# Optimization experiments

Hardware: AMD Instinct MI355X
Metric: run time of the kernel (lower is better)

The kernel has to match this reference:

```python
import math
import jax, jax.numpy as jnp
import numpy as np

EMBED_DIM = 1024
NUM_HEADS = 16
HEAD_DIM = EMBED_DIM // NUM_HEADS  # 64


def setup_inputs() -> dict:
    key = jax.random.key(0)
    kx, kq, ko = jax.random.split(key, 3)
    B, S, D = 4, 1024, EMBED_DIM
    x = jax.random.normal(kx, (B, S, D), dtype=jnp.float32)
    # xavier_uniform for Dense kernels, zeros for biases
    def xavier(k, shape):
        fan_in, fan_out = shape[0], shape[1]
        limit = math.sqrt(6.0 / (fan_in + fan_out))
        return jax.random.uniform(k, shape, jnp.float32, -limit, limit)
    W_qkv = xavier(kq, (D, 3 * D))
    b_qkv = jnp.zeros((3 * D,), jnp.float32)
    W_o = xavier(ko, (D, D))
    b_o = jnp.zeros((D,), jnp.float32)
    return {"x": x, "W_qkv": W_qkv, "b_qkv": b_qkv, "W_o": W_o, "b_o": b_o}


def reference(x, W_qkv, b_qkv, W_o, b_o):
    B, S, D = x.shape
    H, hd = NUM_HEADS, HEAD_DIM
    qkv = x @ W_qkv + b_qkv                         # [B,S,3D]
    qkv = qkv.reshape(B, S, H, 3 * hd).transpose(0, 2, 1, 3)  # [B,H,S,3hd]
    q, k, v = jnp.split(qkv, 3, axis=-1)            # each [B,H,S,hd]
    attn_logits = jnp.einsum('bhqd,bhkd->bhqk', q, k) / math.sqrt(hd)
    attention = jax.nn.softmax(attn_logits, axis=-1)  # [B,H,S,S]
    values = jnp.einsum('bhqk,bhkd->bhqd', attention, v)
    values = values.transpose(0, 2, 1, 3).reshape(B, S, D)
    o = values @ W_o + b_o
    return (o, attention)
```

## Files before the change

kernel.cpp:

```cpp
#include <hip/hip_runtime.h>

#define B_   4
#define S_   1024
#define D_   1024
#define H_   16
#define HD_  64

typedef __bf16 bf16_t;
typedef __attribute__((ext_vector_type(8))) __bf16 bf16x8;
typedef __attribute__((ext_vector_type(4))) float f32x4;

#define MFMA16(a, b, c) __builtin_amdgcn_mfma_f32_16x16x32_bf16((a), (b), (c), 0, 0, 0)

__device__ inline unsigned short f2bf(float f) {
    unsigned int u = __builtin_bit_cast(unsigned int, f);
    u += 0x7FFFu + ((u >> 16) & 1u);
    return (unsigned short)(u >> 16);
}

__device__ inline bf16x8 ld_frag(const unsigned short* p) {
    uint4 u = *(const uint4*)p;
    return __builtin_bit_cast(bf16x8, u);
}

__global__ __launch_bounds__(256) void convert_f32_bf16(
    const float* __restrict__ in, unsigned short* __restrict__ out)
{
    const size_t idx = (size_t)blockIdx.x * 256 + threadIdx.x;
    float4 v = *(const float4*)(in + idx * 4);
    unsigned short* o = out + idx * 4;
    ushort4 r;
    r.x = f2bf(v.x); r.y = f2bf(v.y); r.z = f2bf(v.z); r.w = f2bf(v.w);
    *(ushort4*)o = r;
}

__global__ __launch_bounds__(256) void transpose_f32_bf16(
    const float* __restrict__ in, unsigned short* __restrict__ out,
    int K, int N)
{
    __shared__ float T[64][65];
    const int tid = threadIdx.x;
    const int k0 = blockIdx.y * 64, n0 = blockIdx.x * 64;
#pragma unroll
    for (int i = 0; i < 4; ++i) {
        int c = tid + i * 256;
        int row = c >> 4, col = (c & 15) << 2;
        float4 v = *(const float4*)(in + (size_t)(k0 + row) * N + n0 + col);
        T[row][col + 0] = v.x; T[row][col + 1] = v.y;
        T[row][col + 2] = v.z; T[row][col + 3] = v.w;
    }
    __syncthreads();
#pragma unroll
    for (int i = 0; i < 4; ++i) {
        int c = tid + i * 256;
        int nr = c >> 4, kc = (c & 15) << 2;
        ushort4 r;
        r.x = f2bf(T[kc + 0][nr]); r.y = f2bf(T[kc + 1][nr]);
        r.z = f2bf(T[kc + 2][nr]); r.w = f2bf(T[kc + 3][nr]);
        *(ushort4*)(out + (size_t)(n0 + nr) * K + k0 + kc) = r;
    }
}

template<int MODE>
__global__ __launch_bounds__(256) void gemm_bf16(
    const unsigned short* __restrict__ A,
    const unsigned short* __restrict__ Bt,
    const float* __restrict__ bias,
    unsigned short* __restrict__ qk,
    unsigned short* __restrict__ vt,
    float* __restrict__ out,
    int K, int N)
{
    __shared__ unsigned short Alds[128][72];
    __shared__ unsigned short Blds[128][72];
    const int tid  = threadIdx.x;
    const int l    = tid & 63, w = tid >> 6;
    const int wm   = w >> 1, wn = w & 1;
    const int quad = l >> 4, n16 = l & 15;
    const int bm = blockIdx.y * 128, bn = blockIdx.x * 128;

    const f32x4 zero4 = {0.f, 0.f, 0.f, 0.f};
    f32x4 acc[4][4];
#pragma unroll
    for (int i = 0; i < 4; ++i)
#pragma unroll
        for (int j = 0; j < 4; ++j) acc[i][j] = zero4;

    for (int k0 = 0; k0 < K; k0 += 64) {
#pragma unroll
        for (int i = 0; i < 4; ++i) {
            int c = tid + i * 256;
            int row = c >> 3, off = (c & 7) << 3;
            *(uint4*)&Alds[row][off] = *(const uint4*)(A + (size_t)(bm + row) * K + k0 + off);
            *(uint4*)&Blds[row][off] = *(const uint4*)(Bt + (size_t)(bn + row) * K + k0 + off);
        }
        __syncthreads();
#pragma unroll
        for (int kk = 0; kk < 2; ++kk) {
            const int kc = kk * 32 + quad * 8;
            bf16x8 af[4], bfv[4];
#pragma unroll
            for (int i = 0; i < 4; ++i) af[i]  = ld_frag(&Alds[wm * 64 + i * 16 + n16][kc]);
#pragma unroll
            for (int j = 0; j < 4; ++j) bfv[j] = ld_frag(&Blds[wn * 64 + j * 16 + n16][kc]);
#pragma unroll
            for (int i = 0; i < 4; ++i)
#pragma unroll
                for (int j = 0; j < 4; ++j)
                    acc[i][j] = MFMA16(af[i], bfv[j], acc[i][j]);
        }
        __syncthreads();
    }

#pragma unroll
    for (int j = 0; j < 4; ++j) {
        const int col0 = bn + wn * 64 + j * 16;
        const int col  = col0 + n16;
        const float bv = bias ? bias[col] : 0.f;
        if (MODE == 0) {
            const int head = col0 / 192;
            const int rem  = col0 % 192;
            if (rem < 128) {
#pragma unroll
                for (int i = 0; i < 4; ++i)
#pragma unroll
                    for (int r = 0; r < 4; ++r) {
                        int row = bm + wm * 64 + i * 16 + quad * 4 + r;
                        qk[(size_t)row * 2048 + head * 128 + rem + n16] =
                            f2bf(acc[i][j][r] + bv);
                    }
            } else {
                const int dim = rem - 128 + n16;
#pragma unroll
                for (int i = 0; i < 4; ++i)
#pragma unroll
                    for (int r = 0; r < 4; ++r) {
                        int row = bm + wm * 64 + i * 16 + quad * 4 + r;
                        vt[(size_t)(((row >> 10) << 4) + head) * 65536 +
                           (size_t)dim * 1024 + (row & 1023)] =
                            f2bf(acc[i][j][r] + bv);
                    }
            }
        } else {
#pragma unroll
            for (int i = 0; i < 4; ++i)
#pragma unroll
                for (int r = 0; r < 4; ++r) {
                    int row = bm + wm * 64 + i * 16 + quad * 4 + r;
                    out[(size_t)row * N + col] = acc[i][j][r] + bv;
                }
        }
    }
}

__global__ __launch_bounds__(256) void attn_fused(
    const unsigned short* __restrict__ qk,
    const unsigned short* __restrict__ vt,
    float* __restrict__ attn,
    unsigned short* __restrict__ values)
{
    __shared__ unsigned short Klds[64][72];
    __shared__ unsigned short Vlds[64][72];
    __shared__ unsigned short Plds[16][1032];
    __shared__ float redbuf[2][4][16];

    const int qb = blockIdx.x, bh = blockIdx.y;
    const int b = bh >> 4, h = bh & 15;
    const int tid = threadIdx.x, l = tid & 63, w = tid >> 6;
    const int quad = l >> 4, n16 = l & 15;

    bf16x8 qf[2];
    {
        const unsigned short* qbase =
            qk + (size_t)(b * 1024 + qb * 16 + n16) * 2048 + h * 128 + quad * 8;
        qf[0] = ld_frag(qbase);
        qf[1] = ld_frag(qbase + 32);
    }

    const f32x4 zero4 = {0.f, 0.f, 0.f, 0.f};
    f32x4 c[16];
#pragma unroll
    for (int s = 0; s < 16; ++s) c[s] = zero4;

    const unsigned short* kbase = qk + (size_t)(b * 1024) * 2048 + h * 128 + 64;
    for (int s = 0; s < 16; ++s) {
#pragma unroll
        for (int i = 0; i < 2; ++i) {
            int cc = tid + i * 256;
            int key = cc >> 3, off = (cc & 7) << 3;
            *(uint4*)&Klds[key][off] =
                *(const uint4*)(kbase + (size_t)(s * 64 + key) * 2048 + off);
        }
        __syncthreads();
        const int krow = w * 16 + n16;
        bf16x8 k0f = ld_frag(&Klds[krow][quad * 8]);
        bf16x8 k1f = ld_frag(&Klds[krow][32 + quad * 8]);
        c[s] = MFMA16(qf[0], k0f, c[s]);
        c[s] = MFMA16(qf[1], k1f, c[s]);
        __syncthreads();
    }

    float mx[4] = {-1e30f, -1e30f, -1e30f, -1e30f};
#pragma unroll
    for (int s = 0; s < 16; ++s)
#pragma unroll
        for (int r = 0; r < 4; ++r) {
            c[s][r] *= 0.125f;
            mx[r] = fmaxf(mx[r], c[s][r]);
        }
#pragma unroll
    for (int off = 1; off <= 8; off <<= 1)
#pragma unroll
        for (int r = 0; r < 4; ++r)
            mx[r] = fmaxf(mx[r], __shfl_xor(mx[r], off, 64));
    if (n16 == 0)
#pragma unroll
        for (int r = 0; r < 4; ++r) redbuf[0][w][quad * 4 + r] = mx[r];
    __syncthreads();
#pragma unroll
    for (int r = 0; r < 4; ++r) {
        const int row = quad * 4 + r;
        float m = redbuf[0][0][row];
        m = fmaxf(m, redbuf[0][1][row]);
        m = fmaxf(m, redbuf[0][2][row]);
        m = fmaxf(m, redbuf[0][3][row]);
        mx[r] = m;
    }

    float sm[4] = {0.f, 0.f, 0.f, 0.f};
#pragma unroll
    for (int s = 0; s < 16; ++s)
#pragma unroll
        for (int r = 0; r < 4; ++r) {
            float e = __expf(c[s][r] - mx[r]);
            c[s][r] = e;
            sm[r] += e;
        }
#pragma unroll
    for (int off = 1; off <= 8; off <<= 1)
#pragma unroll
        for (int r = 0; r < 4; ++r)
            sm[r] += __shfl_xor(sm[r], off, 64);
    if (n16 == 0)
#pragma unroll
        for (int r = 0; r < 4; ++r) redbuf[1][w][quad * 4 + r] = sm[r];
    __syncthreads();
    float inv[4];
#pragma unroll
    for (int r = 0; r < 4; ++r) {
        const int row = quad * 4 + r;
        inv[r] = 1.f / (redbuf[1][0][row] + redbuf[1][1][row] +
                        redbuf[1][2][row] + redbuf[1][3][row]);
    }

    float* abase = attn + ((size_t)bh * 1024 + qb * 16) * 1024;
#pragma unroll
    for (int s = 0; s < 16; ++s)
#pragma unroll
        for (int r = 0; r < 4; ++r) {
            const float a = c[s][r] * inv[r];
            const int row = quad * 4 + r;
            const int key = s * 64 + w * 16 + n16;
            abase[(size_t)row * 1024 + key] = a;
            Plds[row][key] = f2bf(a);
        }

    f32x4 o = zero4;
    const unsigned short* vbase = vt + (size_t)bh * 65536;
    for (int s = 0; s < 16; ++s) {
#pragma unroll
        for (int i = 0; i < 2; ++i) {
            int cc = tid + i * 256;
            int dim = cc >> 3, off = (cc & 7) << 3;
            *(uint4*)&Vlds[dim][off] =
                *(const uint4*)(vbase + (size_t)dim * 1024 + s * 64 + off);
        }
        __syncthreads();
#pragma unroll
        for (int kk = 0; kk < 2; ++kk) {
            bf16x8 pf = ld_frag(&Plds[n16][s * 64 + kk * 32 + quad * 8]);
            bf16x8 vf = ld_frag(&Vlds[w * 16 + n16][kk * 32 + quad * 8]);
            o = MFMA16(pf, vf, o);
        }
        __syncthreads();
    }

#pragma unroll
    for (int r = 0; r < 4; ++r) {
        const int row = quad * 4 + r;
        values[(size_t)(b * 1024 + qb * 16 + row) * 1024 + h * 64 + w * 16 + n16] =
            f2bf(o[r]);
    }
}

extern "C" void kernel_launch(void* const* d_in, const int* in_sizes, int n_in,
                              void* d_out, int out_size, void* d_ws, size_t ws_size,
                              hipStream_t stream)
{
    const float* x     = (const float*)d_in[0];
    const float* W_qkv = (const float*)d_in[1];
    const float* b_qkv = (const float*)d_in[2];
    const float* W_o   = (const float*)d_in[3];
    const float* b_o   = (const float*)d_in[4];

    float* o_out    = (float*)d_out;
    float* attn_out = o_out + (size_t)B_ * S_ * D_;

    const size_t M1 = 1ull << 20;
    unsigned short* ws      = (unsigned short*)d_ws;
    unsigned short* x_bf    = ws;
    unsigned short* wqkvt   = ws + 4 * M1;
    unsigned short* wot     = ws + 7 * M1;
    unsigned short* qkbuf   = ws + 8 * M1;
    unsigned short* vtbuf   = ws + 16 * M1;
    unsigned short* valbuf  = ws + 20 * M1;

    convert_f32_bf16<<<4096, 256, 0, stream>>>(x, x_bf);
    transpose_f32_bf16<<<dim3(3072 / 64, 1024 / 64), 256, 0, stream>>>(W_qkv, wqkvt, 1024, 3072);
    transpose_f32_bf16<<<dim3(1024 / 64, 1024 / 64), 256, 0, stream>>>(W_o, wot, 1024, 1024);

    gemm_bf16<0><<<dim3(3072 / 128, 4096 / 128), 256, 0, stream>>>(
        x_bf, wqkvt, b_qkv, qkbuf, vtbuf, nullptr, 1024, 3072);

    attn_fused<<<dim3(S_ / 16, B_ * H_), 256, 0, stream>>>(
        qkbuf, vtbuf, attn_out, valbuf);

    gemm_bf16<1><<<dim3(1024 / 128, 4096 / 128), 256, 0, stream>>>(
        valbuf, wot, b_o, nullptr, nullptr, o_out, 1024, 1024);
}
```

Measured before the change: 477.4 us.

## Use direct global-to-LDS loads in GEMM, double-buffer K/V, split V transpose

The GEMM tile loads now use global_load_lds to write global memory straight into LDS, which removes the register staging and drops the padded LDS rows. The QKV GEMM writes V in its natural layout, and a separate small kernel transposes it into the V^T layout, replacing the scattered strided stores in the GEMM epilogue. The attention kernel double-buffers its K and V tiles so that loading the next tile overlaps compute on the current one, with one barrier per iteration instead of two. The risks are LDS bank conflicts from the unpadded GEMM tiles, an extra kernel launch with its own memory pass for V, and valbuf being reused as scratch for V before the attention kernel overwrites it.

```diff
diff --git a/kernel.cpp b/kernel.cpp
--- a/kernel.cpp
+++ b/kernel.cpp
@@ -21,6 +21,13 @@
 __device__ inline bf16x8 ld_frag(const unsigned short* p) {
     uint4 u = *(const uint4*)p;
     return __builtin_bit_cast(bf16x8, u);
+}
+
+__device__ inline void gload_lds16(const unsigned short* g, unsigned short* l) {
+    __builtin_amdgcn_global_load_lds(
+        (const __attribute__((address_space(1))) void*)g,
+        (__attribute__((address_space(3))) void*)l,
+        16, 0, 0);
 }
 
 __global__ __launch_bounds__(256) void convert_f32_bf16(
@@ -61,24 +68,53 @@
     }
 }
 
+__global__ __launch_bounds__(256) void transpose_v_bf16(
+    const unsigned short* __restrict__ v,
+    unsigned short* __restrict__ vt)
+{
+    __shared__ unsigned short T[64][65];
+    const int tid = threadIdx.x;
+    const int kt = blockIdx.x, bh = blockIdx.y;
+    const int b = bh >> 4, h = bh & 15;
+#pragma unroll
+    for (int i = 0; i < 2; ++i) {
+        const int c = tid + i * 256;
+        const int key = c >> 3, off = (c & 7) << 3;
+        uint4 u = *(const uint4*)(v + (size_t)(b * 1024 + kt * 64 + key) * 1024 + h * 64 + off);
+        union { uint4 u4; unsigned short us[8]; } uu; uu.u4 = u;
+#pragma unroll
+        for (int t = 0; t < 8; ++t) T[key][off + t] = uu.us[t];
+    }
+    __syncthreads();
+#pragma unroll
+    for (int i = 0; i < 16; ++i) {
+        const int c = tid + i * 256;
+        const int dim = c >> 6, key = c & 63;
+        vt[((size_t)bh * 64 + dim) * 1024 + kt * 64 + key] = T[key][dim];
+    }
+}
+
 template<int MODE>
 __global__ __launch_bounds__(256) void gemm_bf16(
     const unsigned short* __restrict__ A,
     const unsigned short* __restrict__ Bt,
     const float* __restrict__ bias,
     unsigned short* __restrict__ qk,
-    unsigned short* __restrict__ vt,
+    unsigned short* __restrict__ vnat,
     float* __restrict__ out,
     int K, int N)
 {
-    __shared__ unsigned short Alds[128][72];
-    __shared__ unsigned short Blds[128][72];
+    __shared__ unsigned short Alds[128][64];
+    __shared__ unsigned short Blds[128][64];
     const int tid  = threadIdx.x;
     const int l    = tid & 63, w = tid >> 6;
     const int wm   = w >> 1, wn = w & 1;
     const int quad = l >> 4, n16 = l & 15;
     const int bm = blockIdx.y * 128, bn = blockIdx.x * 128;
 
+    const int lrow = l >> 3;
+    const int lcol = (l & 7) << 3;
+
     const f32x4 zero4 = {0.f, 0.f, 0.f, 0.f};
     f32x4 acc[4][4];
 #pragma unroll
@@ -89,10 +125,10 @@
     for (int k0 = 0; k0 < K; k0 += 64) {
 #pragma unroll
         for (int i = 0; i < 4; ++i) {
-            int c = tid + i * 256;
-            int row = c >> 3, off = (c & 7) << 3;
-            *(uint4*)&Alds[row][off] = *(const uint4*)(A + (size_t)(bm + row) * K + k0 + off);
-            *(uint4*)&Blds[row][off] = *(const uint4*)(Bt + (size_t)(bn + row) * K + k0 + off);
+            const int c8  = (w * 4 + i) * 8;
+            const int row = c8 + lrow;
+            gload_lds16(A  + (size_t)(bm + row) * K + k0 + lcol, &Alds[c8][0]);
+            gload_lds16(Bt + (size_t)(bn + row) * K + k0 + lcol, &Blds[c8][0]);
         }
         __syncthreads();
 #pragma unroll
@@ -130,15 +166,13 @@
                             f2bf(acc[i][j][r] + bv);
                     }
             } else {
-                const int dim = rem - 128 + n16;
+                const int dcol = head * 64 + (rem - 128) + n16;
 #pragma unroll
                 for (int i = 0; i < 4; ++i)
 #pragma unroll
                     for (int r = 0; r < 4; ++r) {
                         int row = bm + wm * 64 + i * 16 + quad * 4 + r;
-                        vt[(size_t)(((row >> 10) << 4) + head) * 65536 +
-                           (size_t)dim * 1024 + (row & 1023)] =
-                            f2bf(acc[i][j][r] + bv);
+                        vnat[(size_t)row * 1024 + dcol] = f2bf(acc[i][j][r] + bv);
                     }
             }
         } else {
@@ -159,8 +193,7 @@
     float* __restrict__ attn,
     unsigned short* __restrict__ values)
 {
-    __shared__ unsigned short Klds[64][72];
-    __shared__ unsigned short Vlds[64][72];
+    __shared__ unsigned short KV[2][64][72];
     __shared__ unsigned short Plds[16][1032];
     __shared__ float redbuf[2][4][16];
 
@@ -168,6 +201,9 @@
     const int b = bh >> 4, h = bh & 15;
     const int tid = threadIdx.x, l = tid & 63, w = tid >> 6;
     const int quad = l >> 4, n16 = l & 15;
+
+    const int skey = tid >> 3;
+    const int soff = (tid & 7) << 3;
 
     bf16x8 qf[2];
     {
@@ -183,18 +219,23 @@
     for (int s = 0; s < 16; ++s) c[s] = zero4;
 
     const unsigned short* kbase = qk + (size_t)(b * 1024) * 2048 + h * 128 + 64;
+#pragma unroll
+    for (int i = 0; i < 2; ++i)
+        *(uint4*)&KV[0][skey + i * 32][soff] =
+            *(const uint4*)(kbase + (size_t)(skey + i * 32) * 2048 + soff);
+    __syncthreads();
     for (int s = 0; s < 16; ++s) {
-#pragma unroll
-        for (int i = 0; i < 2; ++i) {
-            int cc = tid + i * 256;
-            int key = cc >> 3, off = (cc & 7) << 3;
-            *(uint4*)&Klds[key][off] =
-                *(const uint4*)(kbase + (size_t)(s * 64 + key) * 2048 + off);
-        }
-        __syncthreads();
+        if (s < 15) {
+#pragma unroll
+            for (int i = 0; i < 2; ++i)
+                *(uint4*)&KV[(s + 1) & 1][skey + i * 32][soff] =
+                    *(const uint4*)(kbase +
+                        (size_t)((s + 1) * 64 + skey + i * 32) * 2048 + soff);
+        }
+        const int p = s & 1;
         const int krow = w * 16 + n16;
-        bf16x8 k0f = ld_frag(&Klds[krow][quad * 8]);
-        bf16x8 k1f = ld_frag(&Klds[krow][32 + quad * 8]);
+        bf16x8 k0f = ld_frag(&KV[p][krow][quad * 8]);
+        bf16x8 k1f = ld_frag(&KV[p][krow][32 + quad * 8]);
         c[s] = MFMA16(qf[0], k0f, c[s]);
         c[s] = MFMA16(qf[1], k1f, c[s]);
         __syncthreads();
@@ -267,19 +308,24 @@
 
     f32x4 o = zero4;
     const unsigned short* vbase = vt + (size_t)bh * 65536;
+#pragma unroll
+    for (int i = 0; i < 2; ++i)
+        *(uint4*)&KV[0][skey + i * 32][soff] =
+            *(const uint4*)(vbase + (size_t)(skey + i * 32) * 1024 + soff);
+    __syncthreads();
     for (int s = 0; s < 16; ++s) {
-#pragma unroll
-        for (int i = 0; i < 2; ++i) {
-            int cc = tid + i * 256;
-            int dim = cc >> 3, off = (cc & 7) << 3;
-            *(uint4*)&Vlds[dim][off] =
-                *(const uint4*)(vbase + (size_t)dim * 1024 + s * 64 + off);
-        }
-        __syncthreads();
+        if (s < 15) {
+#pragma unroll
+            for (int i = 0; i < 2; ++i)
+                *(uint4*)&KV[(s + 1) & 1][skey + i * 32][soff] =
+                    *(const uint4*)(vbase +
+                        (size_t)(skey + i * 32) * 1024 + (s + 1) * 64 + soff);
+        }
+        const int p = s & 1;
 #pragma unroll
         for (int kk = 0; kk < 2; ++kk) {
             bf16x8 pf = ld_frag(&Plds[n16][s * 64 + kk * 32 + quad * 8]);
-            bf16x8 vf = ld_frag(&Vlds[w * 16 + n16][kk * 32 + quad * 8]);
+            bf16x8 vf = ld_frag(&KV[p][w * 16 + n16][kk * 32 + quad * 8]);
             o = MFMA16(pf, vf, o);
         }
         __syncthreads();
@@ -320,7 +366,9 @@
     transpose_f32_bf16<<<dim3(1024 / 64, 1024 / 64), 256, 0, stream>>>(W_o, wot, 1024, 1024);
 
     gemm_bf16<0><<<dim3(3072 / 128, 4096 / 128), 256, 0, stream>>>(
-        x_bf, wqkvt, b_qkv, qkbuf, vtbuf, nullptr, 1024, 3072);
+        x_bf, wqkvt, b_qkv, qkbuf, valbuf, nullptr, 1024, 3072);
+
+    transpose_v_bf16<<<dim3(S_ / 64, B_ * H_), 256, 0, stream>>>(valbuf, vtbuf);
 
     attn_fused<<<dim3(S_ / 16, B_ * H_), 256, 0, stream>>>(
         qkbuf, vtbuf, attn_out, valbuf);
```

Result: no change. 486.9 us (+2.0%).
